# Optimization experiments

Hardware: AMD Instinct MI355X
Metric: run time of the kernel (lower is better)

## Reference

```python
import jax, jax.numpy as jnp
import numpy as np

V, E, H = 8192, 1024, 1024  # vocab, embedding_dim, hidden_size (E == H required by the module's math)


def setup_inputs() -> dict:
    key = jax.random.key(0)
    k1, k2, k3, k4, k5 = jax.random.split(key, 5)
    b, l = 32, 512
    x = jax.random.randint(k1, (b, l), 0, V, dtype=jnp.int64)
    hidden = jnp.zeros((b, H), dtype=jnp.float32)
    emb = jax.random.normal(k2, (V, E), dtype=jnp.float32)  # nn.Embedding default init N(0,1)
    W_h = jax.random.normal(k3, (H, H), dtype=jnp.float32) * 0.01
    W_e = jax.random.normal(k4, (H, E), dtype=jnp.float32) * 0.01
    W_o = jax.random.normal(k5, (V, H), dtype=jnp.float32) * 0.01
    return {"x": x, "hidden": hidden, "emb": emb, "W_h": W_h, "W_e": W_e, "W_o": W_o}


def reference(x, hidden, emb, W_h, W_e, W_o):
    # x: [b, l] int ids; hidden: [b, H]
    x_embed = emb[x]                      # [b, l, E]
    x_tl = jnp.swapaxes(x_embed, 0, 1)    # [l, b, E]

    def step(h_prev, x_t):
        h_t = jnp.tanh(x_t @ W_e.T + h_prev @ W_h.T)  # [b, H]
        return h_t, h_t

    final_hidden, outputs = jax.lax.scan(step, hidden, x_tl)  # outputs: [l, b, H]
    outputs = jnp.swapaxes(outputs, 0, 1)                      # [b, l, H]
    logits = outputs @ W_o.T                                   # [b, l, V]
    return logits, final_hidden
```

## Files before the change

kernel.cpp:

```cpp
#include <hip/hip_runtime.h>
#include <math.h>

typedef unsigned short u16;
typedef __attribute__((ext_vector_type(8))) short bf16x8;
typedef __attribute__((ext_vector_type(4))) float f32x4;

#define AS1 __attribute__((address_space(1)))
#define AS3 __attribute__((address_space(3)))

__device__ __forceinline__ void gll16(const u16* g, u16* l) {
  __builtin_amdgcn_global_load_lds((const AS1 void*)g, (AS3 void*)l, 16, 0, 0);
}

__device__ __forceinline__ u16 f2bf(float f) {
  union { float f; unsigned u; } v; v.f = f;
  unsigned r = (v.u + 0x7FFFu + ((v.u >> 16) & 1u)) >> 16;
  return (u16)r;
}

__device__ __forceinline__ float bf2f(u16 h) {
  union { unsigned u; float f; } v; v.u = ((unsigned)h) << 16;
  return v.f;
}

__global__ __launch_bounds__(256) void f32_to_bf16(const float* __restrict__ src,
                                                   u16* __restrict__ dst, int n) {
  int i = blockIdx.x * 256 + threadIdx.x;
  int stride = gridDim.x * 256;
  for (; i < n; i += stride) dst[i] = f2bf(src[i]);
}

__global__ __launch_bounds__(256) void gemm_bt(const u16* __restrict__ A,
                                               const u16* __restrict__ B,
                                               float* __restrict__ C,
                                               int M, int N, int K) {
  __shared__ u16 As[128 * 32];
  __shared__ u16 Bs[128 * 32];
  const int tid  = threadIdx.x;
  const int lane = tid & 63;
  const int wv   = tid >> 6;
  const int quad = lane >> 4;
  const int r16  = lane & 15;
  const int wm   = wv >> 1, wn = wv & 1;
  const int tm   = blockIdx.y, tn = blockIdx.x;
  const int rA   = lane >> 2;
  const int cA   = (lane & 3) * 8;

  f32x4 acc[4][4] = {};
  const size_t Abase = (size_t)(tm * 128) * K;
  const size_t Bbase = (size_t)(tn * 128) * K;

  for (int k0 = 0; k0 < K; k0 += 32) {
#pragma unroll
    for (int q = 0; q < 2; ++q) {
      int r = wv * 32 + q * 16 + rA;
      gll16(A + Abase + (size_t)r * K + k0 + cA, &As[wv * 1024 + q * 512]);
      gll16(B + Bbase + (size_t)r * K + k0 + cA, &Bs[wv * 1024 + q * 512]);
    }
    __syncthreads();
    bf16x8 af[4], bfr[4];
#pragma unroll
    for (int i = 0; i < 4; ++i) {
      af[i]  = *(const bf16x8*)&As[(wm * 64 + i * 16 + r16) * 32 + quad * 8];
      bfr[i] = *(const bf16x8*)&Bs[(wn * 64 + i * 16 + r16) * 32 + quad * 8];
    }
#pragma unroll
    for (int i = 0; i < 4; ++i)
#pragma unroll
      for (int j = 0; j < 4; ++j)
        acc[i][j] = __builtin_amdgcn_mfma_f32_16x16x32_bf16(af[i], bfr[j], acc[i][j], 0, 0, 0);
    __syncthreads();
  }
#pragma unroll
  for (int i = 0; i < 4; ++i) {
    int row = tm * 128 + wm * 64 + i * 16 + quad * 4;
#pragma unroll
    for (int j = 0; j < 4; ++j) {
      int col = tn * 128 + wn * 64 + j * 16 + r16;
#pragma unroll
      for (int r = 0; r < 4; ++r)
        C[(size_t)(row + r) * N + col] = acc[i][j][r];
    }
  }
}

__global__ __launch_bounds__(256) void rnn_step(const u16* __restrict__ Aprev, long Astride,
                                                const u16* __restrict__ Whb,
                                                const float* __restrict__ T,
                                                const int* __restrict__ x, int t,
                                                u16* __restrict__ out_bf) {
  __shared__ u16 As[32 * 256];
  __shared__ u16 Bs[64 * 256];
  const int tid  = threadIdx.x;
  const int lane = tid & 63;
  const int wv   = tid >> 6;
  const int quad = lane >> 4;
  const int r16  = lane & 15;
  const int n0   = blockIdx.x * 64;
  const int rr   = lane >> 5;
  const int cc   = (lane & 31) * 8;

  f32x4 acc[2] = {};

  for (int k0 = 0; k0 < 1024; k0 += 256) {
#pragma unroll
    for (int q = 0; q < 4; ++q) {
      int c = wv * 4 + q;
      int r = 2 * c + rr;
      gll16(Aprev + (size_t)r * Astride + k0 + cc, &As[c * 512]);
    }
#pragma unroll
    for (int q = 0; q < 8; ++q) {
      int c = wv * 8 + q;
      int r = 2 * c + rr;
      gll16(Whb + (size_t)(n0 + r) * 1024 + k0 + cc, &Bs[c * 512]);
    }
    __syncthreads();
#pragma unroll
    for (int kk = 0; kk < 8; ++kk) {
      bf16x8 a0 = *(const bf16x8*)&As[(r16) * 256 + kk * 32 + quad * 8];
      bf16x8 a1 = *(const bf16x8*)&As[(16 + r16) * 256 + kk * 32 + quad * 8];
      bf16x8 b  = *(const bf16x8*)&Bs[(wv * 16 + r16) * 256 + kk * 32 + quad * 8];
      acc[0] = __builtin_amdgcn_mfma_f32_16x16x32_bf16(a0, b, acc[0], 0, 0, 0);
      acc[1] = __builtin_amdgcn_mfma_f32_16x16x32_bf16(a1, b, acc[1], 0, 0, 0);
    }
    __syncthreads();
  }

#pragma unroll
  for (int mt = 0; mt < 2; ++mt) {
    int n = n0 + wv * 16 + r16;
#pragma unroll
    for (int r = 0; r < 4; ++r) {
      int b = mt * 16 + quad * 4 + r;
      int idx = x[b * 512 + t];
      float v = acc[mt][r] + T[(size_t)idx * 1024 + n];
      float h = tanhf(v);
      out_bf[((size_t)b * 512 + t) * 1024 + n] = f2bf(h);
    }
  }
}

__global__ __launch_bounds__(256) void finalize_hidden(const u16* __restrict__ ob,
                                                       float* __restrict__ dst) {
  int i = blockIdx.x * 256 + threadIdx.x;
  int b = i >> 10, j = i & 1023;
  dst[i] = bf2f(ob[((size_t)(b * 512 + 511)) * 1024 + j]);
}

extern "C" void kernel_launch(void* const* d_in, const int* in_sizes, int n_in,
                              void* d_out, int out_size, void* d_ws, size_t ws_size,
                              hipStream_t stream) {
  const int*   x      = (const int*)d_in[0];
  const float* hidden = (const float*)d_in[1];
  const float* emb    = (const float*)d_in[2];
  const float* Wh     = (const float*)d_in[3];
  const float* We     = (const float*)d_in[4];
  const float* Wo     = (const float*)d_in[5];
  float* out = (float*)d_out;

  char* ws = (char*)d_ws;
  u16*   emb_bf = (u16*)(ws);
  u16*   Wo_bf  = (u16*)(ws + 16777216);
  u16*   We_bf  = (u16*)(ws + 33554432);
  u16*   Wh_bf  = (u16*)(ws + 35651584);
  float* T      = (float*)(ws + 37748736);
  u16*   out_bf = (u16*)(ws + 71303168);
  u16*   h_init = (u16*)(ws + 104857600);

  hipLaunchKernelGGL(f32_to_bf16, dim3(2048), dim3(256), 0, stream, emb, emb_bf, 8388608);
  hipLaunchKernelGGL(f32_to_bf16, dim3(2048), dim3(256), 0, stream, Wo, Wo_bf, 8388608);
  hipLaunchKernelGGL(f32_to_bf16, dim3(512),  dim3(256), 0, stream, We, We_bf, 1048576);
  hipLaunchKernelGGL(f32_to_bf16, dim3(512),  dim3(256), 0, stream, Wh, Wh_bf, 1048576);
  hipLaunchKernelGGL(f32_to_bf16, dim3(128),  dim3(256), 0, stream, hidden, h_init, 32768);

  hipLaunchKernelGGL(gemm_bt, dim3(1024 / 128, 8192 / 128), dim3(256), 0, stream,
                     emb_bf, We_bf, T, 8192, 1024, 1024);

  for (int t = 0; t < 512; ++t) {
    const u16* Ap = (t == 0) ? h_init : (out_bf + (size_t)(t - 1) * 1024);
    long Astr = (t == 0) ? 1024L : (512L * 1024L);
    hipLaunchKernelGGL(rnn_step, dim3(16), dim3(256), 0, stream,
                       Ap, Astr, Wh_bf, T, x, t, out_bf);
  }

  hipLaunchKernelGGL(gemm_bt, dim3(8192 / 128, 16384 / 128), dim3(256), 0, stream,
                     out_bf, Wo_bf, out, 16384, 8192, 1024);

  hipLaunchKernelGGL(finalize_hidden, dim3(128), dim3(256), 0, stream,
                     out_bf, out + 134217728);
}
```

Baseline: 7.995 ms.

## Replace per-step RNN launches with persistent scan kernel using global flags

Replaces 512 separate rnn_step launches with one persistent kernel of 32 blocks that loops over time steps and synchronises through per-step atomic counters in global memory. Each thread keeps its slice of W_h in registers across all steps, which removes the repeated reloads of W_h through LDS. Flags live in the output buffer and are cleared by a fused prep kernel, then overwritten later by the logits GEMM. The scheme depends on all 32 blocks being resident at once, and it adds spin-wait and fence latency on every step.

```diff
diff --git a/kernel.cpp b/kernel.cpp
--- a/kernel.cpp
+++ b/kernel.cpp
@@ -28,6 +28,14 @@
   int i = blockIdx.x * 256 + threadIdx.x;
   int stride = gridDim.x * 256;
   for (; i < n; i += stride) dst[i] = f2bf(src[i]);
+}
+
+__global__ __launch_bounds__(256) void prep_h_flags(const float* __restrict__ hidden,
+                                                    u16* __restrict__ h_init,
+                                                    unsigned* __restrict__ flags) {
+  int i = blockIdx.x * 256 + threadIdx.x;
+  if (i < 32768) h_init[i] = f2bf(hidden[i]);
+  if (i < 512) flags[i] = 0u;
 }
 
 __global__ __launch_bounds__(256) void gemm_bt(const u16* __restrict__ A,
@@ -84,60 +92,80 @@
   }
 }
 
-__global__ __launch_bounds__(256) void rnn_step(const u16* __restrict__ Aprev, long Astride,
-                                                const u16* __restrict__ Whb,
-                                                const float* __restrict__ T,
-                                                const int* __restrict__ x, int t,
-                                                u16* __restrict__ out_bf) {
-  __shared__ u16 As[32 * 256];
-  __shared__ u16 Bs[64 * 256];
+#define NBLK 32
+
+__global__ __launch_bounds__(256, 1) void rnn_scan(const u16* __restrict__ h_init,
+                                                   const u16* __restrict__ Whb,
+                                                   const float* __restrict__ T,
+                                                   const int* __restrict__ x,
+                                                   u16* __restrict__ out_bf,
+                                                   unsigned* __restrict__ flags) {
   const int tid  = threadIdx.x;
   const int lane = tid & 63;
   const int wv   = tid >> 6;
   const int quad = lane >> 4;
   const int r16  = lane & 15;
-  const int n0   = blockIdx.x * 64;
-  const int rr   = lane >> 5;
-  const int cc   = (lane & 31) * 8;
-
-  f32x4 acc[2] = {};
-
-  for (int k0 = 0; k0 < 1024; k0 += 256) {
-#pragma unroll
-    for (int q = 0; q < 4; ++q) {
-      int c = wv * 4 + q;
-      int r = 2 * c + rr;
-      gll16(Aprev + (size_t)r * Astride + k0 + cc, &As[c * 512]);
-    }
-#pragma unroll
-    for (int q = 0; q < 8; ++q) {
-      int c = wv * 8 + q;
-      int r = 2 * c + rr;
-      gll16(Whb + (size_t)(n0 + r) * 1024 + k0 + cc, &Bs[c * 512]);
-    }
+  const int wm   = wv >> 1, wn = wv & 1;
+  const int n0   = blockIdx.x * 32;
+  const int n    = n0 + wn * 16 + r16;
+  const int bA   = wm * 16 + r16;
+
+  bf16x8 wr[32];
+  {
+    const u16* wp = Whb + (size_t)n * 1024 + quad * 8;
+#pragma unroll
+    for (int kk = 0; kk < 32; ++kk) wr[kk] = *(const bf16x8*)(wp + kk * 32);
+  }
+
+#pragma unroll 1
+  for (int t = 0; t < 512; ++t) {
+    int idxs[4];
+#pragma unroll
+    for (int r = 0; r < 4; ++r) {
+      int b = wm * 16 + quad * 4 + r;
+      idxs[r] = x[b * 512 + t];
+    }
+    float tv[4];
+#pragma unroll
+    for (int r = 0; r < 4; ++r) tv[r] = T[(size_t)idxs[r] * 1024 + n];
+
+    const u16* hprev;
+    size_t astr;
+    if (t == 0) {
+      hprev = h_init; astr = 1024;
+    } else {
+      hprev = out_bf + (size_t)(t - 1) * 1024; astr = (size_t)512 * 1024;
+      if (tid == 0) {
+        while (__hip_atomic_load(&flags[t - 1], __ATOMIC_RELAXED,
+                                 __HIP_MEMORY_SCOPE_AGENT) < NBLK) {
+          __builtin_amdgcn_s_sleep(1);
+        }
+      }
+      __syncthreads();
+      __threadfence();
+    }
+
+    const u16* ap = hprev + (size_t)bA * astr + quad * 8;
+    bf16x8 a[32];
+#pragma unroll
+    for (int kk = 0; kk < 32; ++kk) a[kk] = *(const bf16x8*)(ap + (size_t)kk * 32);
+
+    f32x4 acc[4] = {};
+#pragma unroll
+    for (int kk = 0; kk < 32; ++kk)
+      acc[kk & 3] = __builtin_amdgcn_mfma_f32_16x16x32_bf16(a[kk], wr[kk], acc[kk & 3], 0, 0, 0);
+
+#pragma unroll
+    for (int r = 0; r < 4; ++r) {
+      int b = wm * 16 + quad * 4 + r;
+      float v = acc[0][r] + acc[1][r] + acc[2][r] + acc[3][r] + tv[r];
+      out_bf[((size_t)b * 512 + t) * 1024 + n] = f2bf(tanhf(v));
+    }
+
+    __threadfence();
     __syncthreads();
-#pragma unroll
-    for (int kk = 0; kk < 8; ++kk) {
-      bf16x8 a0 = *(const bf16x8*)&As[(r16) * 256 + kk * 32 + quad * 8];
-      bf16x8 a1 = *(const bf16x8*)&As[(16 + r16) * 256 + kk * 32 + quad * 8];
-      bf16x8 b  = *(const bf16x8*)&Bs[(wv * 16 + r16) * 256 + kk * 32 + quad * 8];
-      acc[0] = __builtin_amdgcn_mfma_f32_16x16x32_bf16(a0, b, acc[0], 0, 0, 0);
-      acc[1] = __builtin_amdgcn_mfma_f32_16x16x32_bf16(a1, b, acc[1], 0, 0, 0);
-    }
-    __syncthreads();
-  }
-
-#pragma unroll
-  for (int mt = 0; mt < 2; ++mt) {
-    int n = n0 + wv * 16 + r16;
-#pragma unroll
-    for (int r = 0; r < 4; ++r) {
-      int b = mt * 16 + quad * 4 + r;
-      int idx = x[b * 512 + t];
-      float v = acc[mt][r] + T[(size_t)idx * 1024 + n];
-      float h = tanhf(v);
-      out_bf[((size_t)b * 512 + t) * 1024 + n] = f2bf(h);
-    }
+    if (tid == 0)
+      __hip_atomic_fetch_add(&flags[t], 1u, __ATOMIC_RELAXED, __HIP_MEMORY_SCOPE_AGENT);
   }
 }
 
@@ -168,21 +196,19 @@
   u16*   out_bf = (u16*)(ws + 71303168);
   u16*   h_init = (u16*)(ws + 104857600);
 
+  unsigned* flags = (unsigned*)d_out;
+
   hipLaunchKernelGGL(f32_to_bf16, dim3(2048), dim3(256), 0, stream, emb, emb_bf, 8388608);
   hipLaunchKernelGGL(f32_to_bf16, dim3(2048), dim3(256), 0, stream, Wo, Wo_bf, 8388608);
   hipLaunchKernelGGL(f32_to_bf16, dim3(512),  dim3(256), 0, stream, We, We_bf, 1048576);
   hipLaunchKernelGGL(f32_to_bf16, dim3(512),  dim3(256), 0, stream, Wh, Wh_bf, 1048576);
-  hipLaunchKernelGGL(f32_to_bf16, dim3(128),  dim3(256), 0, stream, hidden, h_init, 32768);
+  hipLaunchKernelGGL(prep_h_flags, dim3(128), dim3(256), 0, stream, hidden, h_init, flags);
 
   hipLaunchKernelGGL(gemm_bt, dim3(1024 / 128, 8192 / 128), dim3(256), 0, stream,
                      emb_bf, We_bf, T, 8192, 1024, 1024);
 
-  for (int t = 0; t < 512; ++t) {
-    const u16* Ap = (t == 0) ? h_init : (out_bf + (size_t)(t - 1) * 1024);
-    long Astr = (t == 0) ? 1024L : (512L * 1024L);
-    hipLaunchKernelGGL(rnn_step, dim3(16), dim3(256), 0, stream,
-                       Ap, Astr, Wh_bf, T, x, t, out_bf);
-  }
+  hipLaunchKernelGGL(rnn_scan, dim3(NBLK), dim3(256), 0, stream,
+                     h_init, Wh_bf, T, x, out_bf, flags);
 
   hipLaunchKernelGGL(gemm_bt, dim3(8192 / 128, 16384 / 128), dim3(256), 0, stream,
                      out_bf, Wo_bf, out, 16384, 8192, 1024);
```

After: 6.625 ms. -17.1%, faster.
